# Kernel optimization log

Hardware: AMD Instinct MI355X
Metric: run time of the kernel (lower is better)

Reference implementation:

```python
import jax, jax.numpy as jnp
import numpy as np

V = 50257   # vocab_size
H = 1024    # hidden_size + 8
L = 2048    # input_length
ML = 2048   # max_length


def setup_inputs() -> dict:
    key = jax.random.key(0)
    ks = jax.random.split(key, 12)
    def w(k, shape, scale=0.02):
        return jax.random.normal(k, shape, dtype=jnp.float32) * scale
    return {
        'decoder_input': jax.random.randint(ks[0], (1, 1), 0, V),
        'hidden_state': jax.random.normal(ks[1], (1, 1, H), dtype=jnp.float32),
        'encoder_outputs': jax.random.normal(ks[2], (ML, H), dtype=jnp.float32),
        'input_variable': jax.random.randint(ks[3], (L, 1), 0, V),
        'embedding': w(ks[4], (V, H), 1.0),
        'W_attn_w': w(ks[5], (ML, 2 * H)), 'b_attn_w': jnp.zeros((ML,), jnp.float32),
        'W_attn_u': w(ks[6], (H, 2 * H)), 'b_attn_u': jnp.zeros((H,), jnp.float32),
        'W_ih': w(ks[7], (3 * H, H)), 'b_ih': jnp.zeros((3 * H,), jnp.float32),
        'W_hh': w(ks[8], (3 * H, H)), 'b_hh': jnp.zeros((3 * H,), jnp.float32),
        'W_copy': w(ks[9], (H, H)), 'b_copy': jnp.zeros((H,), jnp.float32),
        'W_gen': w(ks[10], (V, H)), 'b_gen': jnp.zeros((V,), jnp.float32),
    }


def _forward(decoder_input, hidden_state, encoder_outputs, input_variable,
             embedding, W_attn_w, b_attn_w, W_attn_u, b_attn_u,
             W_ih, b_ih, W_hh, b_hh, W_copy, b_copy, W_gen, b_gen):
    # batch_size = 1, single decode step (dropout is identity at inference)
    emb0 = embedding[decoder_input].reshape(1, H)           # (1, H)
    h0 = hidden_state[0]                                    # (1, H) previous hidden

    # attention over encoder outputs
    cat_eh = jnp.concatenate([emb0, h0], axis=1)            # (1, 2H)
    attn_weights = jax.nn.softmax(cat_eh @ W_attn_w.T + b_attn_w, axis=1)  # (1, ML)
    attn_applied = attn_weights @ encoder_outputs           # (1, H)

    joined = jnp.concatenate([emb0, attn_applied], axis=1)  # (1, 2H)
    rnn_in = jax.nn.relu(joined @ W_attn_u.T + b_attn_u)    # (1, H)

    # one GRU step (PyTorch gate layout: r, z, n)
    gi = rnn_in @ W_ih.T + b_ih                             # (1, 3H)
    gh = h0 @ W_hh.T + b_hh                                 # (1, 3H)
    r = jax.nn.sigmoid(gi[:, :H] + gh[:, :H])
    z = jax.nn.sigmoid(gi[:, H:2 * H] + gh[:, H:2 * H])
    n = jnp.tanh(gi[:, 2 * H:] + r * gh[:, 2 * H:])
    h_new = (1.0 - z) * n + z * h0                          # (1, H)
    final_hidden = h_new[None]                              # (1, 1, H)

    # generate + copy scores
    score_g = h_new @ W_gen.T + b_gen                       # (1, V)
    trimmed = encoder_outputs[:L]                           # (L, H)
    score_c = jnp.tanh(trimmed @ W_copy.T + b_copy) @ h0[0] # (L,)  bmm with OLD hidden
    probs = jax.nn.softmax(jnp.concatenate([score_g, score_c[None]], axis=1), axis=1)
    prob_g = probs[:, :V]                                   # (1, V)
    prob_c = probs[:, V:]                                   # (1, L)

    # copy->vocab: scatter-add (math-equivalent to dense one-hot bmm)
    idx = input_variable[:, 0]                              # (L,) int
    prob_c_to_g = jnp.zeros((V,), probs.dtype).at[idx].add(prob_c[0])[None]
    final_output = prob_g + prob_c_to_g                     # (1, V)

    # selective read: attend only to positions matching the current input token
    din = decoder_input[0, 0]
    matched = (idx == din).astype(probs.dtype)              # (L,)
    final_weights = ((prob_c * matched) @ trimmed)[:, None, :]  # (1, 1, H)
    return final_output, final_hidden, final_weights


def reference(decoder_input, hidden_state, encoder_outputs, input_variable,
              embedding, W_attn_w, b_attn_w, W_attn_u, b_attn_u,
              W_ih, b_ih, W_hh, b_hh, W_copy, b_copy, W_gen, b_gen):
    return _forward(decoder_input, hidden_state, encoder_outputs, input_variable,
                    embedding, W_attn_w, b_attn_w, W_attn_u, b_attn_u,
                    W_ih, b_ih, W_hh, b_hh, W_copy, b_copy, W_gen, b_gen)
```

## Files before the change

kernel.cpp:

```cpp
#include <hip/hip_runtime.h>
#include <math.h>

#define VSZ 50257
#define HSZ 1024
#define LSZ 2048
#define SHIFT 60.0f

typedef __attribute__((ext_vector_type(8))) short bf16x8;
typedef __attribute__((ext_vector_type(4))) float f32x4;

__device__ __forceinline__ unsigned short f2bf(float f) {
  unsigned int u = __float_as_uint(f);
  u += 0x7FFFu + ((u >> 16) & 1u);
  return (unsigned short)(u >> 16);
}

__global__ void k_attn(const float* __restrict__ Waw, const float* __restrict__ baw,
                       const int* __restrict__ din, const float* __restrict__ emb,
                       const float* __restrict__ h0, const float* __restrict__ enc,
                       const float* __restrict__ Wc, float* __restrict__ attnw,
                       float* __restrict__ out, float* __restrict__ score_c,
                       float* __restrict__ acc, float* __restrict__ psum,
                       unsigned short* __restrict__ bfbuf) {
  int bid = blockIdx.x, tid = threadIdx.x;
  if (bid < 512) {
    int gw = bid * 4 + (tid >> 6);
    int lane = tid & 63;
    const float4* row = (const float4*)(Waw + (size_t)gw * 2048);
    const float4* e4 = (const float4*)(emb + (size_t)din[0] * HSZ);
    const float4* h4 = (const float4*)h0;
    float s = 0.f;
#pragma unroll
    for (int j = 0; j < 4; ++j) {
      float4 a = row[lane + 64 * j];
      float4 b = e4[lane + 64 * j];
      s += a.x * b.x + a.y * b.y + a.z * b.z + a.w * b.w;
    }
#pragma unroll
    for (int j = 0; j < 4; ++j) {
      float4 a = row[256 + lane + 64 * j];
      float4 b = h4[lane + 64 * j];
      s += a.x * b.x + a.y * b.y + a.z * b.z + a.w * b.w;
    }
#pragma unroll
    for (int o = 32; o > 0; o >>= 1) s += __shfl_down(s, o, 64);
    if (lane == 0) attnw[gw] = s + baw[gw];
  } else if (bid < 709) {
    int v = (bid - 512) * 256 + tid;
    if (v < VSZ) out[v] = 0.f;
  } else if (bid == 709) {
#pragma unroll
    for (int k = 0; k < 8; ++k) score_c[tid + 256 * k] = 0.f;
  } else if (bid == 710) {
#pragma unroll
    for (int k = 0; k < 4; ++k) acc[tid + 256 * k] = 0.f;
    if (tid == 0) psum[0] = 0.f;
  } else {
    int cb = bid - 711;
#pragma unroll
    for (int c = 0; c < 4; ++c) {
      int g = cb * 1024 + c * 256 + tid;
      float4 v;
      if (g < 524288) v = ((const float4*)enc)[g];
      else            v = ((const float4*)Wc)[g - 524288];
      ushort4 o;
      o.x = f2bf(v.x); o.y = f2bf(v.y); o.z = f2bf(v.z); o.w = f2bf(v.w);
      *(ushort4*)(bfbuf + (size_t)g * 4) = o;
    }
  }
}

__global__ void k_attn_apply(const float* __restrict__ attnw, const float* __restrict__ enc,
                             float* __restrict__ acc) {
  __shared__ float red[256];
  __shared__ float sw[64];
  int bid = blockIdx.x, t = threadIdx.x;
  int hb = bid & 3, mb = bid >> 2;
  float m = -1e30f;
  for (int i = t; i < LSZ; i += 256) m = fmaxf(m, attnw[i]);
  red[t] = m; __syncthreads();
  for (int s = 128; s > 0; s >>= 1) { if (t < s) red[t] = fmaxf(red[t], red[t + s]); __syncthreads(); }
  float gmax = red[0]; __syncthreads();
  float sum = 0.f;
  for (int i = t; i < LSZ; i += 256) sum += expf(attnw[i] - gmax);
  red[t] = sum; __syncthreads();
  for (int s = 128; s > 0; s >>= 1) { if (t < s) red[t] += red[t + s]; __syncthreads(); }
  float inv = 1.f / red[0];
  if (t < 64) sw[t] = expf(attnw[mb * 64 + t] - gmax) * inv;
  __syncthreads();
  int h = hb * 256 + t;
  float s = 0.f;
#pragma unroll 4
  for (int j = 0; j < 64; ++j) s = fmaf(sw[j], enc[(size_t)(mb * 64 + j) * HSZ + h], s);
  atomicAdd(&acc[h], s);
}

__global__ void k_rnn(const float* __restrict__ Wau, const float* __restrict__ bau,
                      const int* __restrict__ din, const float* __restrict__ emb,
                      const float* __restrict__ acc, float* __restrict__ rnn_in) {
  int gw = blockIdx.x * 4 + (threadIdx.x >> 6);
  int lane = threadIdx.x & 63;
  const float4* row = (const float4*)(Wau + (size_t)gw * 2048);
  const float4* e4 = (const float4*)(emb + (size_t)din[0] * HSZ);
  const float4* a4 = (const float4*)acc;
  float s = 0.f;
#pragma unroll
  for (int j = 0; j < 4; ++j) {
    float4 a = row[lane + 64 * j];
    float4 b = e4[lane + 64 * j];
    s += a.x * b.x + a.y * b.y + a.z * b.z + a.w * b.w;
  }
#pragma unroll
  for (int j = 0; j < 4; ++j) {
    float4 a = row[256 + lane + 64 * j];
    float4 b = a4[lane + 64 * j];
    s += a.x * b.x + a.y * b.y + a.z * b.z + a.w * b.w;
  }
#pragma unroll
  for (int o = 32; o > 0; o >>= 1) s += __shfl_down(s, o, 64);
  if (lane == 0) rnn_in[gw] = fmaxf(s + bau[gw], 0.f);
}

__global__ void k_gates(const float* __restrict__ Wih, const float* __restrict__ bih,
                        const float* __restrict__ xin, const float* __restrict__ Whh,
                        const float* __restrict__ bhh, const float* __restrict__ h0,
                        float* __restrict__ y) {
  int gw = blockIdx.x * 4 + (threadIdx.x >> 6);
  int lane = threadIdx.x & 63;
  const float* W; const float* x; float bv; int r;
  if (gw < 3 * HSZ) { W = Wih; x = xin; r = gw; bv = bih[r]; }
  else              { W = Whh; x = h0;  r = gw - 3 * HSZ; bv = bhh[r]; }
  const float4* row = (const float4*)(W + (size_t)r * HSZ);
  const float4* xv = (const float4*)x;
  float s = 0.f;
#pragma unroll
  for (int j = 0; j < 4; ++j) {
    float4 a = row[lane + 64 * j];
    float4 b = xv[lane + 64 * j];
    s += a.x * b.x + a.y * b.y + a.z * b.z + a.w * b.w;
  }
#pragma unroll
  for (int o = 32; o > 0; o >>= 1) s += __shfl_down(s, o, 64);
  if (lane == 0) y[gw] = s + bv;
}

__global__ void k_gru(const float* __restrict__ gi, const float* __restrict__ gh,
                      const float* __restrict__ h0, float* __restrict__ h_new,
                      float* __restrict__ out) {
  int t = blockIdx.x * 256 + threadIdx.x;
  float r = 1.f / (1.f + expf(-(gi[t] + gh[t])));
  float z = 1.f / (1.f + expf(-(gi[HSZ + t] + gh[HSZ + t])));
  float n = tanhf(gi[2 * HSZ + t] + r * gh[2 * HSZ + t]);
  float hn = (1.f - z) * n + z * h0[t];
  h_new[t] = hn;
  out[VSZ + t] = hn;
  out[VSZ + HSZ + t] = 0.f;
}

__global__ __launch_bounds__(256) void k_huge(
    const unsigned short* __restrict__ encB, const unsigned short* __restrict__ WcB,
    const float* __restrict__ bc, const float* __restrict__ hvec,
    const float* __restrict__ Wg, const float* __restrict__ bg,
    const float* __restrict__ h_new, float* __restrict__ score) {
  int bid = blockIdx.x, tid = threadIdx.x;
  int wave = tid >> 6, lane = tid & 63;
  if (bid < 512) {
    int l0 = (bid >> 4) * 64 + wave * 16;
    int h0r = (bid & 15) * 64;
    int col = lane & 15, quad = lane >> 4;
    f32x4 acc[4] = {};
    const unsigned short* arow = encB + ((size_t)(l0 + col) << 10) + quad * 8;
#pragma unroll 4
    for (int k0 = 0; k0 < HSZ; k0 += 32) {
      bf16x8 a = *(const bf16x8*)(arow + k0);
#pragma unroll
      for (int ht = 0; ht < 4; ++ht) {
        bf16x8 b = *(const bf16x8*)(WcB + ((size_t)(h0r + ht * 16 + col) << 10) + k0 + quad * 8);
        acc[ht] = __builtin_amdgcn_mfma_f32_16x16x32_bf16(a, b, acc[ht], 0, 0, 0);
      }
    }
    float rsum[4] = {0.f, 0.f, 0.f, 0.f};
#pragma unroll
    for (int ht = 0; ht < 4; ++ht) {
      int h = h0r + ht * 16 + col;
      float bch = bc[h], hw = hvec[h];
#pragma unroll
      for (int r = 0; r < 4; ++r) rsum[r] += tanhf(acc[ht][r] + bch) * hw;
    }
#pragma unroll
    for (int o = 1; o < 16; o <<= 1) {
#pragma unroll
      for (int r = 0; r < 4; ++r) rsum[r] += __shfl_xor(rsum[r], o, 64);
    }
    if (col == 0) {
      int lrow = l0 + quad * 4;
#pragma unroll
      for (int r = 0; r < 4; ++r) atomicAdd(&score[VSZ + lrow + r], rsum[r]);
    }
  } else {
    int r0 = (bid - 512) * 8 + wave * 2;
    int ra = r0 < VSZ ? r0 : VSZ - 1;
    int rb = r0 + 1 < VSZ ? r0 + 1 : VSZ - 1;
    const float4* xv = (const float4*)h_new;
    float4 x0 = xv[lane], x1 = xv[lane + 64], x2 = xv[lane + 128], x3 = xv[lane + 192];
    const float4* p0 = (const float4*)(Wg + (size_t)ra * HSZ);
    const float4* p1 = (const float4*)(Wg + (size_t)rb * HSZ);
    float4 a0 = p0[lane], a1 = p0[lane + 64], a2 = p0[lane + 128], a3 = p0[lane + 192];
    float4 b0 = p1[lane], b1 = p1[lane + 64], b2 = p1[lane + 128], b3 = p1[lane + 192];
    float s0 = a0.x * x0.x + a0.y * x0.y + a0.z * x0.z + a0.w * x0.w
             + a1.x * x1.x + a1.y * x1.y + a1.z * x1.z + a1.w * x1.w
             + a2.x * x2.x + a2.y * x2.y + a2.z * x2.z + a2.w * x2.w
             + a3.x * x3.x + a3.y * x3.y + a3.z * x3.z + a3.w * x3.w;
    float s1 = b0.x * x0.x + b0.y * x0.y + b0.z * x0.z + b0.w * x0.w
             + b1.x * x1.x + b1.y * x1.y + b1.z * x1.z + b1.w * x1.w
             + b2.x * x2.x + b2.y * x2.y + b2.z * x2.z + b2.w * x2.w
             + b3.x * x3.x + b3.y * x3.y + b3.z * x3.z + b3.w * x3.w;
#pragma unroll
    for (int o = 32; o > 0; o >>= 1) {
      s0 += __shfl_down(s0, o, 64);
      s1 += __shfl_down(s1, o, 64);
    }
    if (lane == 0) {
      if (r0 < VSZ) score[r0] = s0 + bg[r0];
      if (r0 + 1 < VSZ) score[r0 + 1] = s1 + bg[r0 + 1];
    }
  }
}

__global__ void k_sum(const float* __restrict__ score, float* __restrict__ psum) {
  __shared__ float sh[256];
  int t = threadIdx.x, b = blockIdx.x;
  float s = 0.f;
  for (int i = b * 256 + t; i < VSZ + LSZ; i += 64 * 256) s += expf(score[i] - SHIFT);
  sh[t] = s; __syncthreads();
  for (int s2 = 128; s2 > 0; s2 >>= 1) { if (t < s2) sh[t] += sh[t + s2]; __syncthreads(); }
  if (t == 0) atomicAdd(psum, sh[0]);
}

__global__ void k_final(const float* __restrict__ score, const float* __restrict__ psum,
                        const int* __restrict__ idx, const int* __restrict__ din,
                        const float* __restrict__ enc, float* __restrict__ out) {
  int bid = blockIdx.x, t = threadIdx.x;
  float inv = 1.f / psum[0];
  if (bid < 197) {
    int v = bid * 256 + t;
    if (v < VSZ) atomicAdd(&out[v], expf(score[v] - SHIFT) * inv);
  } else {
    __shared__ float pm[256];
    __shared__ int flag;
    if (t == 0) flag = 0;
    __syncthreads();
    int l0 = (bid - 197) * 256;
    int l = l0 + t;
    float p = expf(score[VSZ + l] - SHIFT) * inv;
    atomicAdd(&out[idx[l]], p);
    int matched = (idx[l] == din[0]);
    pm[t] = matched ? p : 0.f;
    if (matched) atomicExch(&flag, 1);
    __syncthreads();
    if (flag) {
      for (int h = t; h < HSZ; h += 256) {
        float s = 0.f;
        for (int l2 = 0; l2 < 256; ++l2)
          if (pm[l2] != 0.f) s = fmaf(pm[l2], enc[(size_t)(l0 + l2) * HSZ + h], s);
        if (s != 0.f) atomicAdd(&out[VSZ + HSZ + h], s);
      }
    }
  }
}

extern "C" void kernel_launch(void* const* d_in, const int* in_sizes, int n_in,
                              void* d_out, int out_size, void* d_ws, size_t ws_size,
                              hipStream_t stream) {
  const int*   din = (const int*)d_in[0];
  const float* h0  = (const float*)d_in[1];
  const float* enc = (const float*)d_in[2];
  const int*   idx = (const int*)d_in[3];
  const float* emb = (const float*)d_in[4];
  const float* Waw = (const float*)d_in[5];
  const float* baw = (const float*)d_in[6];
  const float* Wau = (const float*)d_in[7];
  const float* bau = (const float*)d_in[8];
  const float* Wih = (const float*)d_in[9];
  const float* bih = (const float*)d_in[10];
  const float* Whh = (const float*)d_in[11];
  const float* bhh = (const float*)d_in[12];
  const float* Wc  = (const float*)d_in[13];
  const float* bc  = (const float*)d_in[14];
  const float* Wg  = (const float*)d_in[15];
  const float* bg  = (const float*)d_in[16];
  float* out = (float*)d_out;
  float* ws  = (float*)d_ws;

  float* acc    = ws;
  float* rnn_in = ws + 1024;
  float* gi     = ws + 2048;
  float* h_new  = ws + 8192;
  float* attnw  = ws + 9216;
  float* score  = ws + 11264;
  float* psum   = ws + 63616;
  unsigned short* bfbuf = (unsigned short*)(ws + 64000);
  unsigned short* encB = bfbuf;
  unsigned short* WcB  = bfbuf + 2097152;

  k_attn<<<1479, 256, 0, stream>>>(Waw, baw, din, emb, h0, enc, Wc, attnw, out,
                                   score + VSZ, acc, psum, bfbuf);
  k_attn_apply<<<128, 256, 0, stream>>>(attnw, enc, acc);
  k_rnn<<<256, 256, 0, stream>>>(Wau, bau, din, emb, acc, rnn_in);
  k_gates<<<1536, 256, 0, stream>>>(Wih, bih, rnn_in, Whh, bhh, h0, gi);
  k_gru<<<4, 256, 0, stream>>>(gi, gi + 3072, h0, h_new, out);
  k_huge<<<512 + (VSZ + 7) / 8, 256, 0, stream>>>(encB, WcB, bc, h0, Wg, bg, h_new, score);
  k_sum<<<64, 256, 0, stream>>>(score, psum);
  k_final<<<205, 256, 0, stream>>>(score, psum, idx, din, enc, out);
}
```

Before: 462.6 us.

## Fuse GRU into vocab GEMV, prefetch W_gen into cache, fold softmax sum

The GRU cell is recomputed per block inside the vocab projection kernel, and the copy-score MFMA work moves into the gates kernel so it overlaps the gate GEMVs. Extra blocks in the attention-apply and rnn kernels read slices of W_gen and discard the sums, which warms the cache ahead of the vocab GEMV. The exp-sum is accumulated in the vocab kernel, so the separate k_sum launch goes away. The cost is redundant GRU math in every block and prefetch traffic that relies on W_gen staying resident in cache.

```diff
diff --git a/kernel.cpp b/kernel.cpp
--- a/kernel.cpp
+++ b/kernel.cpp
@@ -13,6 +13,14 @@
   unsigned int u = __float_as_uint(f);
   u += 0x7FFFu + ((u >> 16) & 1u);
   return (unsigned short)(u >> 16);
+}
+
+__device__ __forceinline__ float gru1(float gr, float hr, float gz, float hz,
+                                      float gn, float ghn, float h0v) {
+  float r = 1.f / (1.f + expf(-(gr + hr)));
+  float z = 1.f / (1.f + expf(-(gz + hz)));
+  float n = tanhf(gn + r * ghn);
+  return (1.f - z) * n + z * h0v;
 }
 
 __global__ void k_attn(const float* __restrict__ Waw, const float* __restrict__ baw,
@@ -54,6 +62,8 @@
   } else if (bid == 710) {
 #pragma unroll
     for (int k = 0; k < 4; ++k) acc[tid + 256 * k] = 0.f;
+#pragma unroll
+    for (int k = 0; k < 4; ++k) out[VSZ + HSZ + tid + 256 * k] = 0.f;
     if (tid == 0) psum[0] = 0.f;
   } else {
     int cb = bid - 711;
@@ -71,104 +81,113 @@
 }
 
 __global__ void k_attn_apply(const float* __restrict__ attnw, const float* __restrict__ enc,
-                             float* __restrict__ acc) {
-  __shared__ float red[256];
-  __shared__ float sw[64];
+                             float* __restrict__ acc, const float* __restrict__ Wg) {
   int bid = blockIdx.x, t = threadIdx.x;
-  int hb = bid & 3, mb = bid >> 2;
-  float m = -1e30f;
-  for (int i = t; i < LSZ; i += 256) m = fmaxf(m, attnw[i]);
-  red[t] = m; __syncthreads();
-  for (int s = 128; s > 0; s >>= 1) { if (t < s) red[t] = fmaxf(red[t], red[t + s]); __syncthreads(); }
-  float gmax = red[0]; __syncthreads();
-  float sum = 0.f;
-  for (int i = t; i < LSZ; i += 256) sum += expf(attnw[i] - gmax);
-  red[t] = sum; __syncthreads();
-  for (int s = 128; s > 0; s >>= 1) { if (t < s) red[t] += red[t + s]; __syncthreads(); }
-  float inv = 1.f / red[0];
-  if (t < 64) sw[t] = expf(attnw[mb * 64 + t] - gmax) * inv;
-  __syncthreads();
-  int h = hb * 256 + t;
-  float s = 0.f;
-#pragma unroll 4
-  for (int j = 0; j < 64; ++j) s = fmaf(sw[j], enc[(size_t)(mb * 64 + j) * HSZ + h], s);
-  atomicAdd(&acc[h], s);
+  if (bid < 256) {
+    __shared__ float red[256];
+    __shared__ float sw[32];
+    int hb = bid & 3, lb = bid >> 2;
+    float m = -1e30f;
+    for (int i = t; i < LSZ; i += 256) m = fmaxf(m, attnw[i]);
+    red[t] = m; __syncthreads();
+    for (int s = 128; s > 0; s >>= 1) { if (t < s) red[t] = fmaxf(red[t], red[t + s]); __syncthreads(); }
+    float gmax = red[0]; __syncthreads();
+    float sum = 0.f;
+    for (int i = t; i < LSZ; i += 256) sum += expf(attnw[i] - gmax);
+    red[t] = sum; __syncthreads();
+    for (int s = 128; s > 0; s >>= 1) { if (t < s) red[t] += red[t + s]; __syncthreads(); }
+    float inv = 1.f / red[0];
+    if (t < 32) sw[t] = expf(attnw[lb * 32 + t] - gmax) * inv;
+    __syncthreads();
+    int h = hb * 256 + t;
+    float s0 = 0.f, s1 = 0.f, s2 = 0.f, s3 = 0.f;
+#pragma unroll
+    for (int j = 0; j < 32; j += 4) {
+      s0 = fmaf(sw[j + 0], enc[(size_t)(lb * 32 + j + 0) * HSZ + h], s0);
+      s1 = fmaf(sw[j + 1], enc[(size_t)(lb * 32 + j + 1) * HSZ + h], s1);
+      s2 = fmaf(sw[j + 2], enc[(size_t)(lb * 32 + j + 2) * HSZ + h], s2);
+      s3 = fmaf(sw[j + 3], enc[(size_t)(lb * 32 + j + 3) * HSZ + h], s3);
+    }
+    atomicAdd(&acc[h], (s0 + s1) + (s2 + s3));
+  } else {
+    int pb = bid - 256;
+    const float4* wp = (const float4*)Wg + (size_t)pb * 1024;
+    float s = 0.f;
+#pragma unroll
+    for (int c = 0; c < 4; ++c) { float4 v = wp[c * 256 + t]; s += v.x + v.y + v.z + v.w; }
+    asm volatile("" :: "v"(s));
+  }
 }
 
 __global__ void k_rnn(const float* __restrict__ Wau, const float* __restrict__ bau,
                       const int* __restrict__ din, const float* __restrict__ emb,
-                      const float* __restrict__ acc, float* __restrict__ rnn_in) {
-  int gw = blockIdx.x * 4 + (threadIdx.x >> 6);
-  int lane = threadIdx.x & 63;
-  const float4* row = (const float4*)(Wau + (size_t)gw * 2048);
-  const float4* e4 = (const float4*)(emb + (size_t)din[0] * HSZ);
-  const float4* a4 = (const float4*)acc;
-  float s = 0.f;
-#pragma unroll
-  for (int j = 0; j < 4; ++j) {
-    float4 a = row[lane + 64 * j];
-    float4 b = e4[lane + 64 * j];
-    s += a.x * b.x + a.y * b.y + a.z * b.z + a.w * b.w;
-  }
-#pragma unroll
-  for (int j = 0; j < 4; ++j) {
-    float4 a = row[256 + lane + 64 * j];
-    float4 b = a4[lane + 64 * j];
-    s += a.x * b.x + a.y * b.y + a.z * b.z + a.w * b.w;
-  }
-#pragma unroll
-  for (int o = 32; o > 0; o >>= 1) s += __shfl_down(s, o, 64);
-  if (lane == 0) rnn_in[gw] = fmaxf(s + bau[gw], 0.f);
-}
-
-__global__ void k_gates(const float* __restrict__ Wih, const float* __restrict__ bih,
-                        const float* __restrict__ xin, const float* __restrict__ Whh,
-                        const float* __restrict__ bhh, const float* __restrict__ h0,
-                        float* __restrict__ y) {
-  int gw = blockIdx.x * 4 + (threadIdx.x >> 6);
-  int lane = threadIdx.x & 63;
-  const float* W; const float* x; float bv; int r;
-  if (gw < 3 * HSZ) { W = Wih; x = xin; r = gw; bv = bih[r]; }
-  else              { W = Whh; x = h0;  r = gw - 3 * HSZ; bv = bhh[r]; }
-  const float4* row = (const float4*)(W + (size_t)r * HSZ);
-  const float4* xv = (const float4*)x;
-  float s = 0.f;
-#pragma unroll
-  for (int j = 0; j < 4; ++j) {
-    float4 a = row[lane + 64 * j];
-    float4 b = xv[lane + 64 * j];
-    s += a.x * b.x + a.y * b.y + a.z * b.z + a.w * b.w;
-  }
-#pragma unroll
-  for (int o = 32; o > 0; o >>= 1) s += __shfl_down(s, o, 64);
-  if (lane == 0) y[gw] = s + bv;
-}
-
-__global__ void k_gru(const float* __restrict__ gi, const float* __restrict__ gh,
-                      const float* __restrict__ h0, float* __restrict__ h_new,
-                      float* __restrict__ out) {
-  int t = blockIdx.x * 256 + threadIdx.x;
-  float r = 1.f / (1.f + expf(-(gi[t] + gh[t])));
-  float z = 1.f / (1.f + expf(-(gi[HSZ + t] + gh[HSZ + t])));
-  float n = tanhf(gi[2 * HSZ + t] + r * gh[2 * HSZ + t]);
-  float hn = (1.f - z) * n + z * h0[t];
-  h_new[t] = hn;
-  out[VSZ + t] = hn;
-  out[VSZ + HSZ + t] = 0.f;
-}
-
-__global__ __launch_bounds__(256) void k_huge(
+                      const float* __restrict__ acc, float* __restrict__ rnn_in,
+                      const float* __restrict__ Wg) {
+  int bid = blockIdx.x, tid = threadIdx.x;
+  if (bid < 256) {
+    int gw = bid * 4 + (tid >> 6);
+    int lane = tid & 63;
+    const float4* row = (const float4*)(Wau + (size_t)gw * 2048);
+    const float4* e4 = (const float4*)(emb + (size_t)din[0] * HSZ);
+    const float4* a4 = (const float4*)acc;
+    float s = 0.f;
+#pragma unroll
+    for (int j = 0; j < 4; ++j) {
+      float4 a = row[lane + 64 * j];
+      float4 b = e4[lane + 64 * j];
+      s += a.x * b.x + a.y * b.y + a.z * b.z + a.w * b.w;
+    }
+#pragma unroll
+    for (int j = 0; j < 4; ++j) {
+      float4 a = row[256 + lane + 64 * j];
+      float4 b = a4[lane + 64 * j];
+      s += a.x * b.x + a.y * b.y + a.z * b.z + a.w * b.w;
+    }
+#pragma unroll
+    for (int o = 32; o > 0; o >>= 1) s += __shfl_down(s, o, 64);
+    if (lane == 0) rnn_in[gw] = fmaxf(s + bau[gw], 0.f);
+  } else {
+    int pb = bid - 256;
+    const float4* wp = (const float4*)Wg + 786432 + (size_t)pb * 1024;
+    float s = 0.f;
+#pragma unroll
+    for (int c = 0; c < 4; ++c) { float4 v = wp[c * 256 + tid]; s += v.x + v.y + v.z + v.w; }
+    asm volatile("" :: "v"(s));
+  }
+}
+
+__global__ __launch_bounds__(256) void k_gates(
+    const float* __restrict__ Wih, const float* __restrict__ bih,
+    const float* __restrict__ xin, const float* __restrict__ Whh,
+    const float* __restrict__ bhh, const float* __restrict__ h0,
+    float* __restrict__ y,
     const unsigned short* __restrict__ encB, const unsigned short* __restrict__ WcB,
-    const float* __restrict__ bc, const float* __restrict__ hvec,
-    const float* __restrict__ Wg, const float* __restrict__ bg,
-    const float* __restrict__ h_new, float* __restrict__ score) {
+    const float* __restrict__ bc, float* __restrict__ score) {
   int bid = blockIdx.x, tid = threadIdx.x;
   int wave = tid >> 6, lane = tid & 63;
-  if (bid < 512) {
-    int l0 = (bid >> 4) * 64 + wave * 16;
-    int h0r = (bid & 15) * 64;
+  if (bid < 1536) {
+    int gw = bid * 4 + wave;
+    const float* W; const float* x; float bv; int r;
+    if (gw < 3 * HSZ) { W = Wih; x = xin; r = gw; bv = bih[r]; }
+    else              { W = Whh; x = h0;  r = gw - 3 * HSZ; bv = bhh[r]; }
+    const float4* row = (const float4*)(W + (size_t)r * HSZ);
+    const float4* xv = (const float4*)x;
+    float s = 0.f;
+#pragma unroll
+    for (int j = 0; j < 4; ++j) {
+      float4 a = row[lane + 64 * j];
+      float4 b = xv[lane + 64 * j];
+      s += a.x * b.x + a.y * b.y + a.z * b.z + a.w * b.w;
+    }
+#pragma unroll
+    for (int o = 32; o > 0; o >>= 1) s += __shfl_down(s, o, 64);
+    if (lane == 0) y[gw] = s + bv;
+  } else {
+    int g = bid - 1536;
+    int l0 = (g >> 4) * 64 + wave * 16;
+    int h0r = (g & 15) * 64;
     int col = lane & 15, quad = lane >> 4;
-    f32x4 acc[4] = {};
+    f32x4 accf[4] = {};
     const unsigned short* arow = encB + ((size_t)(l0 + col) << 10) + quad * 8;
 #pragma unroll 4
     for (int k0 = 0; k0 < HSZ; k0 += 32) {
@@ -176,16 +195,16 @@
 #pragma unroll
       for (int ht = 0; ht < 4; ++ht) {
         bf16x8 b = *(const bf16x8*)(WcB + ((size_t)(h0r + ht * 16 + col) << 10) + k0 + quad * 8);
-        acc[ht] = __builtin_amdgcn_mfma_f32_16x16x32_bf16(a, b, acc[ht], 0, 0, 0);
+        accf[ht] = __builtin_amdgcn_mfma_f32_16x16x32_bf16(a, b, accf[ht], 0, 0, 0);
       }
     }
     float rsum[4] = {0.f, 0.f, 0.f, 0.f};
 #pragma unroll
     for (int ht = 0; ht < 4; ++ht) {
       int h = h0r + ht * 16 + col;
-      float bch = bc[h], hw = hvec[h];
-#pragma unroll
-      for (int r = 0; r < 4; ++r) rsum[r] += tanhf(acc[ht][r] + bch) * hw;
+      float bch = bc[h], hw = h0[h];
+#pragma unroll
+      for (int r = 0; r < 4; ++r) rsum[r] += tanhf(accf[ht][r] + bch) * hw;
     }
 #pragma unroll
     for (int o = 1; o < 16; o <<= 1) {
@@ -197,44 +216,83 @@
 #pragma unroll
       for (int r = 0; r < 4; ++r) atomicAdd(&score[VSZ + lrow + r], rsum[r]);
     }
-  } else {
-    int r0 = (bid - 512) * 8 + wave * 2;
-    int ra = r0 < VSZ ? r0 : VSZ - 1;
-    int rb = r0 + 1 < VSZ ? r0 + 1 : VSZ - 1;
-    const float4* xv = (const float4*)h_new;
-    float4 x0 = xv[lane], x1 = xv[lane + 64], x2 = xv[lane + 128], x3 = xv[lane + 192];
-    const float4* p0 = (const float4*)(Wg + (size_t)ra * HSZ);
-    const float4* p1 = (const float4*)(Wg + (size_t)rb * HSZ);
-    float4 a0 = p0[lane], a1 = p0[lane + 64], a2 = p0[lane + 128], a3 = p0[lane + 192];
-    float4 b0 = p1[lane], b1 = p1[lane + 64], b2 = p1[lane + 128], b3 = p1[lane + 192];
-    float s0 = a0.x * x0.x + a0.y * x0.y + a0.z * x0.z + a0.w * x0.w
-             + a1.x * x1.x + a1.y * x1.y + a1.z * x1.z + a1.w * x1.w
-             + a2.x * x2.x + a2.y * x2.y + a2.z * x2.z + a2.w * x2.w
-             + a3.x * x3.x + a3.y * x3.y + a3.z * x3.z + a3.w * x3.w;
-    float s1 = b0.x * x0.x + b0.y * x0.y + b0.z * x0.z + b0.w * x0.w
-             + b1.x * x1.x + b1.y * x1.y + b1.z * x1.z + b1.w * x1.w
-             + b2.x * x2.x + b2.y * x2.y + b2.z * x2.z + b2.w * x2.w
-             + b3.x * x3.x + b3.y * x3.y + b3.z * x3.z + b3.w * x3.w;
-#pragma unroll
-    for (int o = 32; o > 0; o >>= 1) {
-      s0 += __shfl_down(s0, o, 64);
-      s1 += __shfl_down(s1, o, 64);
-    }
-    if (lane == 0) {
-      if (r0 < VSZ) score[r0] = s0 + bg[r0];
-      if (r0 + 1 < VSZ) score[r0 + 1] = s1 + bg[r0 + 1];
-    }
-  }
-}
-
-__global__ void k_sum(const float* __restrict__ score, float* __restrict__ psum) {
-  __shared__ float sh[256];
-  int t = threadIdx.x, b = blockIdx.x;
-  float s = 0.f;
-  for (int i = b * 256 + t; i < VSZ + LSZ; i += 64 * 256) s += expf(score[i] - SHIFT);
-  sh[t] = s; __syncthreads();
-  for (int s2 = 128; s2 > 0; s2 >>= 1) { if (t < s2) sh[t] += sh[t + s2]; __syncthreads(); }
-  if (t == 0) atomicAdd(psum, sh[0]);
+  }
+}
+
+__global__ __launch_bounds__(256) void k_vocab(
+    const float* __restrict__ gi, const float* __restrict__ h0,
+    const float* __restrict__ Wg, const float* __restrict__ bg,
+    float* __restrict__ score, float* __restrict__ psum, float* __restrict__ out) {
+  __shared__ float xs[1024];
+  __shared__ float pr[4];
+  int bid = blockIdx.x, tid = threadIdx.x;
+  if (bid >= 6283) {
+    __shared__ float red[256];
+    int l = (bid - 6283) * 256 + tid;
+    red[tid] = expf(score[VSZ + l] - SHIFT);
+    __syncthreads();
+    for (int s = 128; s > 0; s >>= 1) { if (tid < s) red[tid] += red[tid + s]; __syncthreads(); }
+    if (tid == 0) atomicAdd(psum, red[0]);
+    return;
+  }
+  {
+    const float4* G  = (const float4*)gi;
+    const float4* Hh = (const float4*)(gi + 3072);
+    const float4* H0 = (const float4*)h0;
+    float4 gr = G[tid], gz = G[256 + tid], gn = G[512 + tid];
+    float4 hr = Hh[tid], hz = Hh[256 + tid], hn = Hh[512 + tid];
+    float4 h0v = H0[tid];
+    float4 xv;
+    xv.x = gru1(gr.x, hr.x, gz.x, hz.x, gn.x, hn.x, h0v.x);
+    xv.y = gru1(gr.y, hr.y, gz.y, hz.y, gn.y, hn.y, h0v.y);
+    xv.z = gru1(gr.z, hr.z, gz.z, hz.z, gn.z, hn.z, h0v.z);
+    xv.w = gru1(gr.w, hr.w, gz.w, hz.w, gn.w, hn.w, h0v.w);
+    ((float4*)xs)[tid] = xv;
+    if (bid == 0) {
+      int b0 = VSZ + tid * 4;
+      out[b0] = xv.x; out[b0 + 1] = xv.y; out[b0 + 2] = xv.z; out[b0 + 3] = xv.w;
+    }
+  }
+  __syncthreads();
+  int wave = tid >> 6, lane = tid & 63;
+  int r0 = bid * 8 + wave * 2;
+  int ra = r0 < VSZ ? r0 : VSZ - 1;
+  int rb = r0 + 1 < VSZ ? r0 + 1 : VSZ - 1;
+  const float4* xv4 = (const float4*)xs;
+  float4 x0 = xv4[lane], x1 = xv4[lane + 64], x2 = xv4[lane + 128], x3 = xv4[lane + 192];
+  const float4* p0 = (const float4*)(Wg + (size_t)ra * HSZ);
+  const float4* p1 = (const float4*)(Wg + (size_t)rb * HSZ);
+  float4 a0 = p0[lane], a1 = p0[lane + 64], a2 = p0[lane + 128], a3 = p0[lane + 192];
+  float4 b0 = p1[lane], b1 = p1[lane + 64], b2 = p1[lane + 128], b3 = p1[lane + 192];
+  float s0 = a0.x * x0.x + a0.y * x0.y + a0.z * x0.z + a0.w * x0.w
+           + a1.x * x1.x + a1.y * x1.y + a1.z * x1.z + a1.w * x1.w
+           + a2.x * x2.x + a2.y * x2.y + a2.z * x2.z + a2.w * x2.w
+           + a3.x * x3.x + a3.y * x3.y + a3.z * x3.z + a3.w * x3.w;
+  float s1 = b0.x * x0.x + b0.y * x0.y + b0.z * x0.z + b0.w * x0.w
+           + b1.x * x1.x + b1.y * x1.y + b1.z * x1.z + b1.w * x1.w
+           + b2.x * x2.x + b2.y * x2.y + b2.z * x2.z + b2.w * x2.w
+           + b3.x * x3.x + b3.y * x3.y + b3.z * x3.z + b3.w * x3.w;
+#pragma unroll
+  for (int o = 32; o > 0; o >>= 1) {
+    s0 += __shfl_down(s0, o, 64);
+    s1 += __shfl_down(s1, o, 64);
+  }
+  float e = 0.f;
+  if (lane == 0) {
+    if (r0 < VSZ) {
+      float v = s0 + bg[r0];
+      score[r0] = v;
+      e += expf(v - SHIFT);
+    }
+    if (r0 + 1 < VSZ) {
+      float v = s1 + bg[r0 + 1];
+      score[r0 + 1] = v;
+      e += expf(v - SHIFT);
+    }
+    pr[wave] = e;
+  }
+  __syncthreads();
+  if (tid == 0) atomicAdd(psum, (pr[0] + pr[1]) + (pr[2] + pr[3]));
 }
 
 __global__ void k_final(const float* __restrict__ score, const float* __restrict__ psum,
@@ -295,7 +353,6 @@
   float* acc    = ws;
   float* rnn_in = ws + 1024;
   float* gi     = ws + 2048;
-  float* h_new  = ws + 8192;
   float* attnw  = ws + 9216;
   float* score  = ws + 11264;
   float* psum   = ws + 63616;
@@ -305,11 +362,10 @@
 
   k_attn<<<1479, 256, 0, stream>>>(Waw, baw, din, emb, h0, enc, Wc, attnw, out,
                                    score + VSZ, acc, psum, bfbuf);
-  k_attn_apply<<<128, 256, 0, stream>>>(attnw, enc, acc);
-  k_rnn<<<256, 256, 0, stream>>>(Wau, bau, din, emb, acc, rnn_in);
-  k_gates<<<1536, 256, 0, stream>>>(Wih, bih, rnn_in, Whh, bhh, h0, gi);
-  k_gru<<<4, 256, 0, stream>>>(gi, gi + 3072, h0, h_new, out);
-  k_huge<<<512 + (VSZ + 7) / 8, 256, 0, stream>>>(encB, WcB, bc, h0, Wg, bg, h_new, score);
-  k_sum<<<64, 256, 0, stream>>>(score, psum);
+  k_attn_apply<<<1024, 256, 0, stream>>>(attnw, enc, acc, Wg);
+  k_rnn<<<1024, 256, 0, stream>>>(Wau, bau, din, emb, acc, rnn_in, Wg);
+  k_gates<<<2048, 256, 0, stream>>>(Wih, bih, rnn_in, Whh, bhh, h0, gi,
+                                    encB, WcB, bc, score);
+  k_vocab<<<6291, 256, 0, stream>>>(gi, h0, Wg, bg, score, psum, out);
   k_final<<<205, 256, 0, stream>>>(score, psum, idx, din, enc, out);
 }
```

After: 522.5 us. 1.13x slower.

## Fuse GRU update and softmax sum into preceding kernels via last-block atomics

Applied to the files above, without the earlier changes.

Removes the separate k_gru and k_sum launches. The GRU elementwise step now runs in the last block to finish k_gates, which it detects with an atomic counter and threadfence. The generator rows now add their exp-sum contributions to psum directly, and the last block of k_huge adds the copy-score part. This cuts two launches and one full pass over the scores, at the cost of an extra atomic per block and a serialized tail block.

```diff
diff --git a/kernel.cpp b/kernel.cpp
--- a/kernel.cpp
+++ b/kernel.cpp
@@ -13,6 +13,14 @@
   unsigned int u = __float_as_uint(f);
   u += 0x7FFFu + ((u >> 16) & 1u);
   return (unsigned short)(u >> 16);
+}
+
+__device__ __forceinline__ float gru1(float gr, float hr, float gz, float hz,
+                                      float gn, float ghn, float h0v) {
+  float r = 1.f / (1.f + expf(-(gr + hr)));
+  float z = 1.f / (1.f + expf(-(gz + hz)));
+  float n = tanhf(gn + r * ghn);
+  return (1.f - z) * n + z * h0v;
 }
 
 __global__ void k_attn(const float* __restrict__ Waw, const float* __restrict__ baw,
@@ -21,7 +29,7 @@
                        const float* __restrict__ Wc, float* __restrict__ attnw,
                        float* __restrict__ out, float* __restrict__ score_c,
                        float* __restrict__ acc, float* __restrict__ psum,
-                       unsigned short* __restrict__ bfbuf) {
+                       int* __restrict__ cnts, unsigned short* __restrict__ bfbuf) {
   int bid = blockIdx.x, tid = threadIdx.x;
   if (bid < 512) {
     int gw = bid * 4 + (tid >> 6);
@@ -54,7 +62,9 @@
   } else if (bid == 710) {
 #pragma unroll
     for (int k = 0; k < 4; ++k) acc[tid + 256 * k] = 0.f;
-    if (tid == 0) psum[0] = 0.f;
+#pragma unroll
+    for (int k = 0; k < 4; ++k) out[VSZ + HSZ + tid + 256 * k] = 0.f;
+    if (tid == 0) { psum[0] = 0.f; cnts[0] = 0; cnts[1] = 0; }
   } else {
     int cb = bid - 711;
 #pragma unroll
@@ -124,9 +134,11 @@
 __global__ void k_gates(const float* __restrict__ Wih, const float* __restrict__ bih,
                         const float* __restrict__ xin, const float* __restrict__ Whh,
                         const float* __restrict__ bhh, const float* __restrict__ h0,
-                        float* __restrict__ y) {
-  int gw = blockIdx.x * 4 + (threadIdx.x >> 6);
-  int lane = threadIdx.x & 63;
+                        float* __restrict__ y, float* __restrict__ h_new,
+                        float* __restrict__ out, int* __restrict__ cnt) {
+  int bid = blockIdx.x, tid = threadIdx.x;
+  int gw = bid * 4 + (tid >> 6);
+  int lane = tid & 63;
   const float* W; const float* x; float bv; int r;
   if (gw < 3 * HSZ) { W = Wih; x = xin; r = gw; bv = bih[r]; }
   else              { W = Whh; x = h0;  r = gw - 3 * HSZ; bv = bhh[r]; }
@@ -142,33 +154,44 @@
 #pragma unroll
   for (int o = 32; o > 0; o >>= 1) s += __shfl_down(s, o, 64);
   if (lane == 0) y[gw] = s + bv;
-}
-
-__global__ void k_gru(const float* __restrict__ gi, const float* __restrict__ gh,
-                      const float* __restrict__ h0, float* __restrict__ h_new,
-                      float* __restrict__ out) {
-  int t = blockIdx.x * 256 + threadIdx.x;
-  float r = 1.f / (1.f + expf(-(gi[t] + gh[t])));
-  float z = 1.f / (1.f + expf(-(gi[HSZ + t] + gh[HSZ + t])));
-  float n = tanhf(gi[2 * HSZ + t] + r * gh[2 * HSZ + t]);
-  float hn = (1.f - z) * n + z * h0[t];
-  h_new[t] = hn;
-  out[VSZ + t] = hn;
-  out[VSZ + HSZ + t] = 0.f;
+  __shared__ int lastf;
+  __syncthreads();
+  if (tid == 0) { __threadfence(); lastf = (atomicAdd(cnt, 1) == 1535); }
+  __syncthreads();
+  if (lastf) {
+    __threadfence();
+    const float4* G  = (const float4*)y;
+    const float4* Hh = (const float4*)(y + 3072);
+    const float4* H0 = (const float4*)h0;
+    float4 gr = G[tid], gz = G[256 + tid], gn = G[512 + tid];
+    float4 hr = Hh[tid], hz = Hh[256 + tid], hn4 = Hh[512 + tid];
+    float4 h0v = H0[tid];
+    float4 xo;
+    xo.x = gru1(gr.x, hr.x, gz.x, hz.x, gn.x, hn4.x, h0v.x);
+    xo.y = gru1(gr.y, hr.y, gz.y, hz.y, gn.y, hn4.y, h0v.y);
+    xo.z = gru1(gr.z, hr.z, gz.z, hz.z, gn.z, hn4.z, h0v.z);
+    xo.w = gru1(gr.w, hr.w, gz.w, hz.w, gn.w, hn4.w, h0v.w);
+    ((float4*)h_new)[tid] = xo;
+    int b0 = VSZ + tid * 4;
+    out[b0] = xo.x; out[b0 + 1] = xo.y; out[b0 + 2] = xo.z; out[b0 + 3] = xo.w;
+  }
 }
 
 __global__ __launch_bounds__(256) void k_huge(
     const unsigned short* __restrict__ encB, const unsigned short* __restrict__ WcB,
     const float* __restrict__ bc, const float* __restrict__ hvec,
     const float* __restrict__ Wg, const float* __restrict__ bg,
-    const float* __restrict__ h_new, float* __restrict__ score) {
+    const float* __restrict__ h_new, float* __restrict__ score,
+    float* __restrict__ psum, int* __restrict__ cnt) {
   int bid = blockIdx.x, tid = threadIdx.x;
   int wave = tid >> 6, lane = tid & 63;
+  __shared__ float pr[4];
+  __shared__ int lastf;
   if (bid < 512) {
     int l0 = (bid >> 4) * 64 + wave * 16;
     int h0r = (bid & 15) * 64;
     int col = lane & 15, quad = lane >> 4;
-    f32x4 acc[4] = {};
+    f32x4 accf[4] = {};
     const unsigned short* arow = encB + ((size_t)(l0 + col) << 10) + quad * 8;
 #pragma unroll 4
     for (int k0 = 0; k0 < HSZ; k0 += 32) {
@@ -176,7 +199,7 @@
 #pragma unroll
       for (int ht = 0; ht < 4; ++ht) {
         bf16x8 b = *(const bf16x8*)(WcB + ((size_t)(h0r + ht * 16 + col) << 10) + k0 + quad * 8);
-        acc[ht] = __builtin_amdgcn_mfma_f32_16x16x32_bf16(a, b, acc[ht], 0, 0, 0);
+        accf[ht] = __builtin_amdgcn_mfma_f32_16x16x32_bf16(a, b, accf[ht], 0, 0, 0);
       }
     }
     float rsum[4] = {0.f, 0.f, 0.f, 0.f};
@@ -185,7 +208,7 @@
       int h = h0r + ht * 16 + col;
       float bch = bc[h], hw = hvec[h];
 #pragma unroll
-      for (int r = 0; r < 4; ++r) rsum[r] += tanhf(acc[ht][r] + bch) * hw;
+      for (int r = 0; r < 4; ++r) rsum[r] += tanhf(accf[ht][r] + bch) * hw;
     }
 #pragma unroll
     for (int o = 1; o < 16; o <<= 1) {
@@ -221,20 +244,34 @@
       s1 += __shfl_down(s1, o, 64);
     }
     if (lane == 0) {
-      if (r0 < VSZ) score[r0] = s0 + bg[r0];
-      if (r0 + 1 < VSZ) score[r0 + 1] = s1 + bg[r0 + 1];
-    }
-  }
-}
-
-__global__ void k_sum(const float* __restrict__ score, float* __restrict__ psum) {
-  __shared__ float sh[256];
-  int t = threadIdx.x, b = blockIdx.x;
-  float s = 0.f;
-  for (int i = b * 256 + t; i < VSZ + LSZ; i += 64 * 256) s += expf(score[i] - SHIFT);
-  sh[t] = s; __syncthreads();
-  for (int s2 = 128; s2 > 0; s2 >>= 1) { if (t < s2) sh[t] += sh[t + s2]; __syncthreads(); }
-  if (t == 0) atomicAdd(psum, sh[0]);
+      float e = 0.f;
+      if (r0 < VSZ) {
+        float v = s0 + bg[r0];
+        score[r0] = v;
+        e += expf(v - SHIFT);
+      }
+      if (r0 + 1 < VSZ) {
+        float v = s1 + bg[r0 + 1];
+        score[r0 + 1] = v;
+        e += expf(v - SHIFT);
+      }
+      pr[wave] = e;
+    }
+    __syncthreads();
+    if (tid == 0) atomicAdd(psum, (pr[0] + pr[1]) + (pr[2] + pr[3]));
+  }
+  __syncthreads();
+  if (tid == 0) { __threadfence(); lastf = (atomicAdd(cnt, 1) == 512 + 6283 - 1); }
+  __syncthreads();
+  if (lastf) {
+    __threadfence();
+    __shared__ float red[256];
+    float e = 0.f;
+    for (int l = tid; l < LSZ; l += 256) e += expf(score[VSZ + l] - SHIFT);
+    red[tid] = e; __syncthreads();
+    for (int s2 = 128; s2 > 0; s2 >>= 1) { if (tid < s2) red[tid] += red[tid + s2]; __syncthreads(); }
+    if (tid == 0) atomicAdd(psum, red[0]);
+  }
 }
 
 __global__ void k_final(const float* __restrict__ score, const float* __restrict__ psum,
@@ -299,17 +336,18 @@
   float* attnw  = ws + 9216;
   float* score  = ws + 11264;
   float* psum   = ws + 63616;
+  int*   cnts   = (int*)(ws + 63620);
   unsigned short* bfbuf = (unsigned short*)(ws + 64000);
   unsigned short* encB = bfbuf;
   unsigned short* WcB  = bfbuf + 2097152;
 
   k_attn<<<1479, 256, 0, stream>>>(Waw, baw, din, emb, h0, enc, Wc, attnw, out,
-                                   score + VSZ, acc, psum, bfbuf);
+                                   score + VSZ, acc, psum, cnts, bfbuf);
   k_attn_apply<<<128, 256, 0, stream>>>(attnw, enc, acc);
   k_rnn<<<256, 256, 0, stream>>>(Wau, bau, din, emb, acc, rnn_in);
-  k_gates<<<1536, 256, 0, stream>>>(Wih, bih, rnn_in, Whh, bhh, h0, gi);
-  k_gru<<<4, 256, 0, stream>>>(gi, gi + 3072, h0, h_new, out);
-  k_huge<<<512 + (VSZ + 7) / 8, 256, 0, stream>>>(encB, WcB, bc, h0, Wg, bg, h_new, score);
-  k_sum<<<64, 256, 0, stream>>>(score, psum);
+  k_gates<<<1536, 256, 0, stream>>>(Wih, bih, rnn_in, Whh, bhh, h0, gi, h_new, out,
+                                    cnts + 0);
+  k_huge<<<512 + (VSZ + 7) / 8, 256, 0, stream>>>(encB, WcB, bc, h0, Wg, bg, h_new,
+                                                  score, psum, cnts + 1);
   k_final<<<205, 256, 0, stream>>>(score, psum, idx, din, enc, out);
 }
```

Result: slower. 813.0 us (+75.7%).
